# Kernel tuning notes

Measured on AMD Instinct MI355X. Metric: run time of the kernel, lower is better.

The kernel has to match this reference:

```python
import jax, jax.numpy as jnp
import numpy as np

D_MODEL = 1024
N_HEADS = 16
D_K = D_MODEL // N_HEADS
B, L = 2, 2048


def setup_inputs() -> dict:
    key = jax.random.key(0)
    ks = jax.random.split(key, 13)
    s = 0.02
    inp = {
        'query': jax.random.normal(ks[0], (B, L, D_MODEL), jnp.float32),
        'key': jax.random.normal(ks[1], (B, L, D_MODEL), jnp.float32),
        'value': jax.random.normal(ks[2], (B, L, D_MODEL), jnp.float32),
        'mask': jax.random.randint(ks[3], (1, 1, L, L), 0, 2).astype(bool),
        'W_q': jax.random.normal(ks[4], (D_MODEL, D_MODEL), jnp.float32) * s,
        'b_q': jnp.zeros((D_MODEL,), jnp.float32),
        'W_k': jax.random.normal(ks[5], (D_MODEL, D_MODEL), jnp.float32) * s,
        'b_k': jnp.zeros((D_MODEL,), jnp.float32),
        'W_v': jax.random.normal(ks[6], (D_MODEL, D_MODEL), jnp.float32) * s,
        'b_v': jnp.zeros((D_MODEL,), jnp.float32),
        'W_o': jax.random.normal(ks[7], (D_MODEL, D_MODEL), jnp.float32) * s,
        'b_o': jnp.zeros((D_MODEL,), jnp.float32),
    }
    return inp


def _split_heads(x):
    b, l, _ = x.shape
    return x.reshape(b, l, N_HEADS, D_K).transpose(0, 2, 1, 3)  # [B,H,L,dk]


def reference(query, key, value, mask, W_q, b_q, W_k, b_k, W_v, b_v, W_o, b_o):
    q = _split_heads(query @ W_q + b_q)
    k = _split_heads(key @ W_k + b_k)
    v = _split_heads(value @ W_v + b_v)
    # Unscaled attention logits [B,H,L,L] (NO 1/sqrt(dk))
    logits = jnp.einsum('bhqd,bhkd->bhqk', q, k)
    logits = jnp.where(mask, -jnp.inf, logits)
    w = jax.nn.softmax(logits, axis=-1)
    w = jnp.nan_to_num(w, nan=0.0)  # fully-masked rows -> zeros
    attended = jnp.einsum('bhqk,bhkd->bhqd', w, v)
    # dropout in eval mode = identity; combine heads
    out = attended.transpose(0, 2, 1, 3).reshape(B, L, D_MODEL)
    return out @ W_o + b_o
```

## Files before the change

### kernel.cpp

```cpp
#include <hip/hip_runtime.h>
#include <hip/hip_bf16.h>
#include <stdint.h>


typedef __bf16 bf16;
typedef __bf16 bf16x8 __attribute__((ext_vector_type(8)));
typedef float f32x4 __attribute__((ext_vector_type(4)));

#define AS1 __attribute__((address_space(1)))
#define AS3 __attribute__((address_space(3)))

__device__ __forceinline__ void g2l16(const void* g, void* l) {
    __builtin_amdgcn_global_load_lds((AS1 void*)g, (AS3 void*)l, 16, 0, 0);
}

__device__ __forceinline__ bool lane_masked(unsigned long long m) {
#if __has_builtin(__builtin_amdgcn_inverse_ballot_w64)
    return __builtin_amdgcn_inverse_ballot_w64(m);
#else
    return (m >> (threadIdx.x & 63)) & 1ull;
#endif
}

#define LOG2E 1.44269504088896f

__global__ __launch_bounds__(256) void cvt3_kernel(const float* __restrict__ a0,
                                                   const float* __restrict__ a1,
                                                   const float* __restrict__ a2,
                                                   bf16* o0, bf16* o1, bf16* o2) {
    int y = blockIdx.y;
    const float* in = (y == 0) ? a0 : (y == 1) ? a1 : a2;
    bf16* out = (y == 0) ? o0 : (y == 1) ? o1 : o2;
    int idx = blockIdx.x * 256 + threadIdx.x;
    float4 v = ((const float4*)in)[idx];
    __align__(8) bf16 o[4];
    o[0] = (bf16)v.x; o[1] = (bf16)v.y; o[2] = (bf16)v.z; o[3] = (bf16)v.w;
    *(uint2*)(out + (size_t)idx * 4) = *(const uint2*)o;
}

__global__ __launch_bounds__(256) void mdetect_kernel(const unsigned int* __restrict__ w,
                                                      int* __restrict__ flag) {
    int idx = blockIdx.x * 256 + threadIdx.x;
    unsigned v = w[idx];
    int f = 0;
    if (v == 0x3F800000u) f = 2;
    else if (v > 1u) f = 1;
    unsigned long long b1 = __ballot(f & 1);
    unsigned long long b2 = __ballot(f & 2);
    if ((threadIdx.x & 63) == 0) {
        int agg = (b1 ? 1 : 0) | (b2 ? 2 : 0);
        if (agg) atomicOr(flag, agg);
    }
}

__global__ __launch_bounds__(256) void mpack_kernel(const void* __restrict__ mask,
                                                    unsigned long long* __restrict__ mb,
                                                    const int* __restrict__ flag) {
    int idx = blockIdx.x * 256 + threadIdx.x;
    int f = *flag;
    bool v;
    if (f & 2)      v = ((const float*)mask)[idx] != 0.0f;
    else if (f & 1) v = ((const unsigned char*)mask)[idx] != 0;
    else            v = ((const int*)mask)[idx] != 0;
    unsigned long long b = __ballot(v);
    if ((threadIdx.x & 63) == 0) mb[idx >> 6] = b;
}

__global__ __launch_bounds__(256) void rpack_kernel(const unsigned long long* __restrict__ mb,
                                                    unsigned long long* __restrict__ rmb) {
    int task = blockIdx.x * 4 + (threadIdx.x >> 6);
    int qg = task >> 5, kt = task & 31;
    int lane = threadIdx.x & 63, quad = lane >> 4, col = lane & 15;
    #pragma unroll
    for (int r = 0; r < 4; ++r) {
        unsigned long long wrow = mb[(size_t)(qg * 16 + quad * 4 + r) * 32 + kt];
        #pragma unroll
        for (int nt = 0; nt < 4; ++nt) {
            unsigned long long b = __ballot(((wrow >> (nt * 16 + col)) & 1ull) != 0);
            if (lane == 0) rmb[(size_t)task * 16 + r * 4 + nt] = b;
        }
    }
}

__global__ __launch_bounds__(256) void wtrans_kernel(const float* W0, const float* W1,
                                                     const float* W2, const float* W3,
                                                     bf16* T0, bf16* T1, bf16* T2, bf16* T3) {
    const float* W; bf16* T;
    int y = blockIdx.y;
    if (y == 0)      { W = W0; T = T0; }
    else if (y == 1) { W = W1; T = T1; }
    else if (y == 2) { W = W2; T = T2; }
    else             { W = W3; T = T3; }
    int tx = blockIdx.x & 15, ty = blockIdx.x >> 4;
    int n0 = tx * 64, k0 = ty * 64;
    __shared__ __align__(16) bf16 t[64 * 72];
    int tid = threadIdx.x;
    #pragma unroll
    for (int rr = 0; rr < 4; ++rr) {
        int idx = rr * 256 + tid;
        int r = idx >> 4, c4 = (idx & 15) * 4;
        float4 v = *(const float4*)(W + (size_t)(k0 + r) * 1024 + n0 + c4);
        __align__(8) bf16 o[4];
        o[0] = (bf16)v.x; o[1] = (bf16)v.y; o[2] = (bf16)v.z; o[3] = (bf16)v.w;
        *(uint2*)&t[r * 72 + c4] = *(const uint2*)o;
    }
    __syncthreads();
    #pragma unroll
    for (int rr = 0; rr < 2; ++rr) {
        int idx = rr * 256 + tid;
        int n = idx >> 3, kc = (idx & 7) * 8;
        __align__(16) bf16 o[8];
        #pragma unroll
        for (int j = 0; j < 8; ++j) o[j] = t[(kc + j) * 72 + n];
        *(uint4*)(T + (size_t)(n0 + n) * 1024 + k0 + kc) = *(const uint4*)o;
    }
}

template <int MODE>
__device__ __forceinline__ void gemm128_core(const bf16* __restrict__ A,
                                             const bf16* __restrict__ Bt,
                                             const float* __restrict__ bias,
                                             void* __restrict__ Out, int bm, int bn,
                                             float scale) {
    __shared__ __align__(16) bf16 la[128 * 32];
    __shared__ __align__(16) bf16 lb[128 * 32];
    int tid = threadIdx.x;
    int w = tid >> 6, lane = tid & 63;
    int quad = lane >> 4, col = lane & 15;
    int wm = w >> 1, wn = w & 1;
    int m0 = bm * 128, n0 = bn * 128;
    f32x4 acc[4][4];
    f32x4 z = {0.f, 0.f, 0.f, 0.f};
    #pragma unroll
    for (int i = 0; i < 4; ++i)
        #pragma unroll
        for (int j = 0; j < 4; ++j) acc[i][j] = z;
    int srow = lane >> 2;
    int skc = (lane & 3) * 8;
    for (int kt = 0; kt < 32; ++kt) {
        int kk = kt * 32;
        __syncthreads();
        #pragma unroll
        for (int rr = 0; rr < 2; ++rr) {
            int ch = rr * 4 + w;
            int row = ch * 16 + srow;
            g2l16(A + (size_t)(m0 + row) * 1024 + kk + skc, &la[ch * 512]);
            g2l16(Bt + (size_t)(n0 + row) * 1024 + kk + skc, &lb[ch * 512]);
        }
        __syncthreads();
        bf16x8 af[4], bfr[4];
        #pragma unroll
        for (int mt = 0; mt < 4; ++mt)
            af[mt] = *(const bf16x8*)&la[(wm * 64 + mt * 16 + col) * 32 + quad * 8];
        #pragma unroll
        for (int nt = 0; nt < 4; ++nt)
            bfr[nt] = *(const bf16x8*)&lb[(wn * 64 + nt * 16 + col) * 32 + quad * 8];
        #pragma unroll
        for (int mt = 0; mt < 4; ++mt)
            #pragma unroll
            for (int nt = 0; nt < 4; ++nt)
                acc[mt][nt] = __builtin_amdgcn_mfma_f32_16x16x32_bf16(
                    af[mt], bfr[nt], acc[mt][nt], 0, 0, 0);
    }
    float bia[4];
    #pragma unroll
    for (int nt = 0; nt < 4; ++nt) bia[nt] = bias[n0 + wn * 64 + nt * 16 + col];
    #pragma unroll
    for (int mt = 0; mt < 4; ++mt) {
        #pragma unroll
        for (int nt = 0; nt < 4; ++nt) {
            #pragma unroll
            for (int r = 0; r < 4; ++r) {
                int m = m0 + wm * 64 + mt * 16 + quad * 4 + r;
                int n = n0 + wn * 64 + nt * 16 + col;
                float v = (acc[mt][nt][r] + bia[nt]) * scale;
                if (MODE == 0) {
                    int b = m >> 11, l = m & 2047, h = n >> 6, d = n & 63;
                    ((bf16*)Out)[(((size_t)b * 16 + h) * 2048 + l) * 64 + d] = (bf16)v;
                } else {
                    int b = m >> 11, l = m & 2047, h = n >> 6, d = n & 63;
                    ((bf16*)Out)[(((size_t)b * 16 + h) * 64 + d) * 2048 + l] = (bf16)v;
                }
            }
        }
    }
}

__global__ __launch_bounds__(256) void qkv_kernel(
    const bf16* Xq, const bf16* Xk, const bf16* Xv,
    const bf16* Wq, const bf16* Wk, const bf16* Wv,
    const float* bq, const float* bk, const float* bv,
    bf16* Qh, bf16* Kh, bf16* Vt) {
    int y = blockIdx.y;
    int bm = blockIdx.x >> 3, bn = blockIdx.x & 7;
    if (y == 0)      gemm128_core<0>(Xq, Wq, bq, Qh, bm, bn, LOG2E);
    else if (y == 1) gemm128_core<0>(Xk, Wk, bk, Kh, bm, bn, 1.0f);
    else             gemm128_core<2>(Xv, Wv, bv, Vt, bm, bn, 1.0f);
}

__global__ __launch_bounds__(256) void ogemm_kernel(const bf16* __restrict__ A,
                                                    const bf16* __restrict__ Wt,
                                                    const float* __restrict__ bias,
                                                    float* __restrict__ Out) {
    int bm = blockIdx.x >> 3, bn = blockIdx.x & 7;
    __shared__ __align__(16) bf16 la[64 * 32];
    __shared__ __align__(16) bf16 lb[128 * 32];
    int tid = threadIdx.x;
    int w = tid >> 6, lane = tid & 63;
    int quad = lane >> 4, col = lane & 15;
    int m0 = bm * 64, n0 = bn * 128;
    f32x4 acc[4][2];
    f32x4 z = {0.f, 0.f, 0.f, 0.f};
    #pragma unroll
    for (int i = 0; i < 4; ++i) { acc[i][0] = z; acc[i][1] = z; }
    int srow = lane >> 2;
    int skc = (lane & 3) * 8;
    for (int kt = 0; kt < 32; ++kt) {
        int kk = kt * 32;
        __syncthreads();
        g2l16(A + (size_t)(m0 + w * 16 + srow) * 1024 + kk + skc, &la[w * 512]);
        #pragma unroll
        for (int rr = 0; rr < 2; ++rr) {
            int ch = rr * 4 + w;
            g2l16(Wt + (size_t)(n0 + ch * 16 + srow) * 1024 + kk + skc, &lb[ch * 512]);
        }
        __syncthreads();
        bf16x8 af[4], bfr[2];
        #pragma unroll
        for (int mt = 0; mt < 4; ++mt)
            af[mt] = *(const bf16x8*)&la[(mt * 16 + col) * 32 + quad * 8];
        #pragma unroll
        for (int nt = 0; nt < 2; ++nt)
            bfr[nt] = *(const bf16x8*)&lb[(w * 32 + nt * 16 + col) * 32 + quad * 8];
        #pragma unroll
        for (int mt = 0; mt < 4; ++mt)
            #pragma unroll
            for (int nt = 0; nt < 2; ++nt)
                acc[mt][nt] = __builtin_amdgcn_mfma_f32_16x16x32_bf16(
                    af[mt], bfr[nt], acc[mt][nt], 0, 0, 0);
    }
    float bia[2];
    bia[0] = bias[n0 + w * 32 + col];
    bia[1] = bias[n0 + w * 32 + 16 + col];
    #pragma unroll
    for (int mt = 0; mt < 4; ++mt)
        #pragma unroll
        for (int nt = 0; nt < 2; ++nt)
            #pragma unroll
            for (int r = 0; r < 4; ++r)
                Out[(size_t)(m0 + mt * 16 + quad * 4 + r) * 1024 +
                    n0 + w * 32 + nt * 16 + col] = acc[mt][nt][r] + bia[nt];
}

__global__ __launch_bounds__(128) void attn_kernel(const bf16* __restrict__ Qh,
                                                   const bf16* __restrict__ Kh,
                                                   const bf16* __restrict__ Vt,
                                                   const unsigned long long* __restrict__ rmb,
                                                   bf16* __restrict__ att) {
    int bh = blockIdx.x, qt = blockIdx.y;
    int b = bh >> 4, h = bh & 15;
    int q0 = qt * 64;
    __shared__ __align__(16) bf16 ks[64 * 64];
    __shared__ __align__(16) bf16 vs[64 * 64];
    __shared__ __align__(16) bf16 ps[2 * 32 * 72];
    int tid = threadIdx.x;
    int w = tid >> 6, lane = tid & 63;
    int quad = lane >> 4, col = lane & 15;
    int c7 = col & 7;
    int sr = lane >> 3;
    int sg = (lane & 7) ^ sr;
    int swz0 = (quad ^ c7) * 8;
    int swz1 = ((4 + quad) ^ c7) * 8;

    int mofs = __builtin_amdgcn_readfirstlane((qt * 4 + w * 2) * 512);

    #pragma unroll
    for (int i = 0; i < 4; ++i) {
        int ch = w * 4 + i;
        g2l16(Qh + ((size_t)bh * 2048 + q0 + ch * 8 + sr) * 64 + sg * 8, &ks[ch * 512]);
    }
    __syncthreads();
    bf16x8 aq[2][2];
    #pragma unroll
    for (int mt = 0; mt < 2; ++mt) {
        aq[mt][0] = *(const bf16x8*)&ks[(w * 32 + mt * 16 + col) * 64 + swz0];
        aq[mt][1] = *(const bf16x8*)&ks[(w * 32 + mt * 16 + col) * 64 + swz1];
    }
    bf16x8 onesf;
    #pragma unroll
    for (int i = 0; i < 8; ++i) onesf[i] = (bf16)1.0f;

    f32x4 z = {0.f, 0.f, 0.f, 0.f};
    f32x4 O[2][4], R[2];
    #pragma unroll
    for (int mt = 0; mt < 2; ++mt) {
        R[mt] = z;
        #pragma unroll
        for (int i = 0; i < 4; ++i) O[mt][i] = z;
    }

    for (int kt = 0; kt < 32; ++kt) {
        __syncthreads();
        #pragma unroll
        for (int i = 0; i < 4; ++i) {
            int ch = w * 4 + i;
            int r = ch * 8 + sr;
            g2l16(Kh + ((size_t)bh * 2048 + kt * 64 + r) * 64 + sg * 8, &ks[ch * 512]);
            g2l16(Vt + ((size_t)bh * 64 + r) * 2048 + kt * 64 + sg * 8, &vs[ch * 512]);
        }
        __syncthreads();

        f32x4 s[2][4];
        #pragma unroll
        for (int nt = 0; nt < 4; ++nt) {
            s[0][nt] = z; s[1][nt] = z;
            bf16x8 bk0 = *(const bf16x8*)&ks[(nt * 16 + col) * 64 + swz0];
            s[0][nt] = __builtin_amdgcn_mfma_f32_16x16x32_bf16(aq[0][0], bk0, s[0][nt], 0, 0, 0);
            s[1][nt] = __builtin_amdgcn_mfma_f32_16x16x32_bf16(aq[1][0], bk0, s[1][nt], 0, 0, 0);
            bf16x8 bk1 = *(const bf16x8*)&ks[(nt * 16 + col) * 64 + swz1];
            s[0][nt] = __builtin_amdgcn_mfma_f32_16x16x32_bf16(aq[0][1], bk1, s[0][nt], 0, 0, 0);
            s[1][nt] = __builtin_amdgcn_mfma_f32_16x16x32_bf16(aq[1][1], bk1, s[1][nt], 0, 0, 0);
        }

        #pragma unroll
        for (int mt = 0; mt < 2; ++mt) {
            const unsigned long long* mw = rmb + mofs + mt * 512 + kt * 16;
            #pragma unroll
            for (int r = 0; r < 4; ++r) {
                #pragma unroll
                for (int nt = 0; nt < 4; ++nt) {
                    float p = __builtin_amdgcn_exp2f(s[mt][nt][r]);
                    if (lane_masked(mw[r * 4 + nt])) p = 0.0f;
                    ps[w * 2304 + (mt * 16 + quad * 4 + r) * 72 + nt * 16 + col] = (bf16)p;
                }
            }
        }

        bf16x8 ap[2][2];
        #pragma unroll
        for (int mt = 0; mt < 2; ++mt) {
            ap[mt][0] = *(const bf16x8*)&ps[w * 2304 + (mt * 16 + col) * 72 + quad * 8];
            ap[mt][1] = *(const bf16x8*)&ps[w * 2304 + (mt * 16 + col) * 72 + 32 + quad * 8];
        }
        #pragma unroll
        for (int dt = 0; dt < 4; ++dt) {
            bf16x8 bv0 = *(const bf16x8*)&vs[(dt * 16 + col) * 64 + swz0];
            O[0][dt] = __builtin_amdgcn_mfma_f32_16x16x32_bf16(ap[0][0], bv0, O[0][dt], 0, 0, 0);
            O[1][dt] = __builtin_amdgcn_mfma_f32_16x16x32_bf16(ap[1][0], bv0, O[1][dt], 0, 0, 0);
            bf16x8 bv1 = *(const bf16x8*)&vs[(dt * 16 + col) * 64 + swz1];
            O[0][dt] = __builtin_amdgcn_mfma_f32_16x16x32_bf16(ap[0][1], bv1, O[0][dt], 0, 0, 0);
            O[1][dt] = __builtin_amdgcn_mfma_f32_16x16x32_bf16(ap[1][1], bv1, O[1][dt], 0, 0, 0);
        }
        #pragma unroll
        for (int mt = 0; mt < 2; ++mt) {
            R[mt] = __builtin_amdgcn_mfma_f32_16x16x32_bf16(ap[mt][0], onesf, R[mt], 0, 0, 0);
            R[mt] = __builtin_amdgcn_mfma_f32_16x16x32_bf16(ap[mt][1], onesf, R[mt], 0, 0, 0);
        }
    }

    #pragma unroll
    for (int mt = 0; mt < 2; ++mt) {
        #pragma unroll
        for (int r = 0; r < 4; ++r) {
            float rsv = R[mt][r];
            float inv = (rsv > 0.f) ? 1.0f / rsv : 0.f;
            int qg = q0 + w * 32 + mt * 16 + quad * 4 + r;
            #pragma unroll
            for (int dt = 0; dt < 4; ++dt) {
                float ov = O[mt][dt][r] * inv;
                att[((size_t)b * 2048 + qg) * 1024 + h * 64 + dt * 16 + col] = (bf16)ov;
            }
        }
    }
}

extern "C" void kernel_launch(void* const* d_in, const int* in_sizes, int n_in,
                              void* d_out, int out_size, void* d_ws, size_t ws_size,
                              hipStream_t stream) {
    (void)in_sizes; (void)n_in; (void)out_size; (void)ws_size;
    const float* query = (const float*)d_in[0];
    const float* key_  = (const float*)d_in[1];
    const float* value = (const float*)d_in[2];
    const void*  mask  = d_in[3];
    const float* W_q = (const float*)d_in[4];
    const float* b_q = (const float*)d_in[5];
    const float* W_k = (const float*)d_in[6];
    const float* b_k = (const float*)d_in[7];
    const float* W_v = (const float*)d_in[8];
    const float* b_v = (const float*)d_in[9];
    const float* W_o = (const float*)d_in[10];
    const float* b_o = (const float*)d_in[11];

    char* ws = (char*)d_ws;
    bf16* Xq  = (bf16*)(ws + 0);
    bf16* Xk  = (bf16*)(ws + 8388608);
    bf16* Xv  = (bf16*)(ws + 16777216);
    bf16* Wtq = (bf16*)(ws + 25165824);
    bf16* Wtk = (bf16*)(ws + 27262976);
    bf16* Wtv = (bf16*)(ws + 29360128);
    bf16* Wto = (bf16*)(ws + 31457280);
    bf16* Qh  = (bf16*)(ws + 33554432);
    bf16* Kh  = (bf16*)(ws + 41943040);
    bf16* Vt  = (bf16*)(ws + 50331648);
    bf16* att = (bf16*)(ws + 58720256);
    unsigned long long* mb  = (unsigned long long*)(ws + 67108864);
    unsigned long long* rmb = (unsigned long long*)(ws + 67633152);
    int* flag = (int*)(ws + 68157440);

    hipMemsetAsync(flag, 0, 4, stream);
    mdetect_kernel<<<4096, 256, 0, stream>>>((const unsigned int*)mask, flag);
    mpack_kernel<<<16384, 256, 0, stream>>>(mask, mb, flag);
    rpack_kernel<<<1024, 256, 0, stream>>>(mb, rmb);

    cvt3_kernel<<<dim3(4096, 3), 256, 0, stream>>>(query, key_, value, Xq, Xk, Xv);
    wtrans_kernel<<<dim3(256, 4), 256, 0, stream>>>(W_q, W_k, W_v, W_o, Wtq, Wtk, Wtv, Wto);

    qkv_kernel<<<dim3(256, 3), 256, 0, stream>>>(Xq, Xk, Xv, Wtq, Wtk, Wtv,
                                                 b_q, b_k, b_v, Qh, Kh, Vt);
    attn_kernel<<<dim3(32, 32), 128, 0, stream>>>(Qh, Kh, Vt, rmb, att);
    ogemm_kernel<<<512, 256, 0, stream>>>(att, Wto, b_o, (float*)d_out);
}
```

Baseline: 274.3 us.

## Split attention key range across two wave pairs and merge partial results in LDS

The attention kernel now runs 256 threads per block. Two halves of the block each process half of the key sequence in 32-key tiles, and their partial O and row-sum accumulators are reduced through shared memory at the end. The aim is more waves per block and more latency hiding for the same grid size, which doubles the parallelism along the key dimension. In exchange it adds a final LDS reduction, smaller per-iteration tiles with more barriers per unit of work, and changed V tile swizzling and mask indexing.

```diff
diff --git a/kernel.cpp b/kernel.cpp
--- a/kernel.cpp
+++ b/kernel.cpp
@@ -252,7 +252,7 @@
                     n0 + w * 32 + nt * 16 + col] = acc[mt][nt][r] + bia[nt];
 }
 
-__global__ __launch_bounds__(128) void attn_kernel(const bf16* __restrict__ Qh,
+__global__ __launch_bounds__(256) void attn_kernel(const bf16* __restrict__ Qh,
                                                    const bf16* __restrict__ Kh,
                                                    const bf16* __restrict__ Vt,
                                                    const unsigned long long* __restrict__ rmb,
@@ -260,31 +260,34 @@
     int bh = blockIdx.x, qt = blockIdx.y;
     int b = bh >> 4, h = bh & 15;
     int q0 = qt * 64;
-    __shared__ __align__(16) bf16 ks[64 * 64];
-    __shared__ __align__(16) bf16 vs[64 * 64];
-    __shared__ __align__(16) bf16 ps[2 * 32 * 72];
+    __shared__ __align__(16) bf16 kv[2][2][32 * 64];
+    __shared__ __align__(16) bf16 ps[4][32 * 36];
     int tid = threadIdx.x;
     int w = tid >> 6, lane = tid & 63;
+    int half = w >> 1, wq = w & 1;
     int quad = lane >> 4, col = lane & 15;
-    int c7 = col & 7;
+    int c7 = col & 7, c3 = col & 3;
     int sr = lane >> 3;
     int sg = (lane & 7) ^ sr;
+    int vr = lane >> 2;
+    int vg = (lane & 3) ^ (vr & 3);
     int swz0 = (quad ^ c7) * 8;
     int swz1 = ((4 + quad) ^ c7) * 8;
 
-    int mofs = __builtin_amdgcn_readfirstlane((qt * 4 + w * 2) * 512);
-
-    #pragma unroll
-    for (int i = 0; i < 4; ++i) {
-        int ch = w * 4 + i;
-        g2l16(Qh + ((size_t)bh * 2048 + q0 + ch * 8 + sr) * 64 + sg * 8, &ks[ch * 512]);
+    int mofs = __builtin_amdgcn_readfirstlane((qt * 4 + wq * 2) * 512);
+
+    bf16* qb = &kv[0][0][0];
+    #pragma unroll
+    for (int i = 0; i < 2; ++i) {
+        int ch = w * 2 + i;
+        g2l16(Qh + ((size_t)bh * 2048 + q0 + ch * 8 + sr) * 64 + sg * 8, qb + ch * 512);
     }
     __syncthreads();
     bf16x8 aq[2][2];
     #pragma unroll
     for (int mt = 0; mt < 2; ++mt) {
-        aq[mt][0] = *(const bf16x8*)&ks[(w * 32 + mt * 16 + col) * 64 + swz0];
-        aq[mt][1] = *(const bf16x8*)&ks[(w * 32 + mt * 16 + col) * 64 + swz1];
+        aq[mt][0] = *(const bf16x8*)&qb[(wq * 32 + mt * 16 + col) * 64 + swz0];
+        aq[mt][1] = *(const bf16x8*)&qb[(wq * 32 + mt * 16 + col) * 64 + swz1];
     }
     bf16x8 onesf;
     #pragma unroll
@@ -299,76 +302,93 @@
         for (int i = 0; i < 4; ++i) O[mt][i] = z;
     }
 
-    for (int kt = 0; kt < 32; ++kt) {
-        __syncthreads();
-        #pragma unroll
-        for (int i = 0; i < 4; ++i) {
-            int ch = w * 4 + i;
-            int r = ch * 8 + sr;
-            g2l16(Kh + ((size_t)bh * 2048 + kt * 64 + r) * 64 + sg * 8, &ks[ch * 512]);
-            g2l16(Vt + ((size_t)bh * 64 + r) * 2048 + kt * 64 + sg * 8, &vs[ch * 512]);
-        }
-        __syncthreads();
-
-        f32x4 s[2][4];
-        #pragma unroll
-        for (int nt = 0; nt < 4; ++nt) {
+    bf16* ksb = &kv[half][0][0];
+    bf16* vsb = &kv[half][1][0];
+    for (int it = 0; it < 32; ++it) {
+        int kt = half * 32 + it;
+        __syncthreads();
+        #pragma unroll
+        for (int i = 0; i < 2; ++i) {
+            int ch = wq * 2 + i;
+            g2l16(Kh + ((size_t)bh * 2048 + kt * 32 + ch * 8 + sr) * 64 + sg * 8,
+                  ksb + ch * 512);
+            g2l16(Vt + ((size_t)bh * 64 + ch * 16 + vr) * 2048 + kt * 32 + vg * 8,
+                  vsb + ch * 512);
+        }
+        __syncthreads();
+
+        f32x4 s[2][2];
+        #pragma unroll
+        for (int nt = 0; nt < 2; ++nt) {
             s[0][nt] = z; s[1][nt] = z;
-            bf16x8 bk0 = *(const bf16x8*)&ks[(nt * 16 + col) * 64 + swz0];
+            bf16x8 bk0 = *(const bf16x8*)&ksb[(nt * 16 + col) * 64 + swz0];
             s[0][nt] = __builtin_amdgcn_mfma_f32_16x16x32_bf16(aq[0][0], bk0, s[0][nt], 0, 0, 0);
             s[1][nt] = __builtin_amdgcn_mfma_f32_16x16x32_bf16(aq[1][0], bk0, s[1][nt], 0, 0, 0);
-            bf16x8 bk1 = *(const bf16x8*)&ks[(nt * 16 + col) * 64 + swz1];
+            bf16x8 bk1 = *(const bf16x8*)&ksb[(nt * 16 + col) * 64 + swz1];
             s[0][nt] = __builtin_amdgcn_mfma_f32_16x16x32_bf16(aq[0][1], bk1, s[0][nt], 0, 0, 0);
             s[1][nt] = __builtin_amdgcn_mfma_f32_16x16x32_bf16(aq[1][1], bk1, s[1][nt], 0, 0, 0);
         }
 
         #pragma unroll
         for (int mt = 0; mt < 2; ++mt) {
-            const unsigned long long* mw = rmb + mofs + mt * 512 + kt * 16;
+            const unsigned long long* mw =
+                rmb + mofs + mt * 512 + (kt >> 1) * 16 + (kt & 1) * 2;
             #pragma unroll
             for (int r = 0; r < 4; ++r) {
                 #pragma unroll
-                for (int nt = 0; nt < 4; ++nt) {
+                for (int nt = 0; nt < 2; ++nt) {
                     float p = __builtin_amdgcn_exp2f(s[mt][nt][r]);
                     if (lane_masked(mw[r * 4 + nt])) p = 0.0f;
-                    ps[w * 2304 + (mt * 16 + quad * 4 + r) * 72 + nt * 16 + col] = (bf16)p;
+                    ps[w][(mt * 16 + quad * 4 + r) * 36 + nt * 16 + col] = (bf16)p;
                 }
             }
         }
 
-        bf16x8 ap[2][2];
+        bf16x8 ap[2];
+        ap[0] = *(const bf16x8*)&ps[w][(col) * 36 + quad * 8];
+        ap[1] = *(const bf16x8*)&ps[w][(16 + col) * 36 + quad * 8];
+        #pragma unroll
+        for (int dt = 0; dt < 4; ++dt) {
+            bf16x8 bv = *(const bf16x8*)&vsb[(dt * 16 + col) * 32 + (quad ^ c3) * 8];
+            O[0][dt] = __builtin_amdgcn_mfma_f32_16x16x32_bf16(ap[0], bv, O[0][dt], 0, 0, 0);
+            O[1][dt] = __builtin_amdgcn_mfma_f32_16x16x32_bf16(ap[1], bv, O[1][dt], 0, 0, 0);
+        }
+        R[0] = __builtin_amdgcn_mfma_f32_16x16x32_bf16(ap[0], onesf, R[0], 0, 0, 0);
+        R[1] = __builtin_amdgcn_mfma_f32_16x16x32_bf16(ap[1], onesf, R[1], 0, 0, 0);
+    }
+
+    __syncthreads();
+    float* obuf = (float*)&kv[0][0][0];
+    float* rbuf = (float*)&ps[0][0];
+    if (half == 1) {
         #pragma unroll
         for (int mt = 0; mt < 2; ++mt) {
-            ap[mt][0] = *(const bf16x8*)&ps[w * 2304 + (mt * 16 + col) * 72 + quad * 8];
-            ap[mt][1] = *(const bf16x8*)&ps[w * 2304 + (mt * 16 + col) * 72 + 32 + quad * 8];
-        }
-        #pragma unroll
-        for (int dt = 0; dt < 4; ++dt) {
-            bf16x8 bv0 = *(const bf16x8*)&vs[(dt * 16 + col) * 64 + swz0];
-            O[0][dt] = __builtin_amdgcn_mfma_f32_16x16x32_bf16(ap[0][0], bv0, O[0][dt], 0, 0, 0);
-            O[1][dt] = __builtin_amdgcn_mfma_f32_16x16x32_bf16(ap[1][0], bv0, O[1][dt], 0, 0, 0);
-            bf16x8 bv1 = *(const bf16x8*)&vs[(dt * 16 + col) * 64 + swz1];
-            O[0][dt] = __builtin_amdgcn_mfma_f32_16x16x32_bf16(ap[0][1], bv1, O[0][dt], 0, 0, 0);
-            O[1][dt] = __builtin_amdgcn_mfma_f32_16x16x32_bf16(ap[1][1], bv1, O[1][dt], 0, 0, 0);
-        }
+            #pragma unroll
+            for (int r = 0; r < 4; ++r) {
+                int row = mt * 16 + quad * 4 + r;
+                #pragma unroll
+                for (int dt = 0; dt < 4; ++dt)
+                    obuf[(size_t)wq * 2048 + row * 64 + dt * 16 + col] = O[mt][dt][r];
+                if (col == 0) rbuf[wq * 32 + row] = R[mt][r];
+            }
+        }
+    }
+    __syncthreads();
+    if (half == 0) {
         #pragma unroll
         for (int mt = 0; mt < 2; ++mt) {
-            R[mt] = __builtin_amdgcn_mfma_f32_16x16x32_bf16(ap[mt][0], onesf, R[mt], 0, 0, 0);
-            R[mt] = __builtin_amdgcn_mfma_f32_16x16x32_bf16(ap[mt][1], onesf, R[mt], 0, 0, 0);
-        }
-    }
-
-    #pragma unroll
-    for (int mt = 0; mt < 2; ++mt) {
-        #pragma unroll
-        for (int r = 0; r < 4; ++r) {
-            float rsv = R[mt][r];
-            float inv = (rsv > 0.f) ? 1.0f / rsv : 0.f;
-            int qg = q0 + w * 32 + mt * 16 + quad * 4 + r;
-            #pragma unroll
-            for (int dt = 0; dt < 4; ++dt) {
-                float ov = O[mt][dt][r] * inv;
-                att[((size_t)b * 2048 + qg) * 1024 + h * 64 + dt * 16 + col] = (bf16)ov;
+            #pragma unroll
+            for (int r = 0; r < 4; ++r) {
+                int row = mt * 16 + quad * 4 + r;
+                float rsv = R[mt][r] + rbuf[wq * 32 + row];
+                float inv = (rsv > 0.f) ? 1.0f / rsv : 0.f;
+                int qg = q0 + wq * 32 + row;
+                #pragma unroll
+                for (int dt = 0; dt < 4; ++dt) {
+                    float ov = (O[mt][dt][r] +
+                                obuf[(size_t)wq * 2048 + row * 64 + dt * 16 + col]) * inv;
+                    att[((size_t)b * 2048 + qg) * 1024 + h * 64 + dt * 16 + col] = (bf16)ov;
+                }
             }
         }
     }
@@ -417,6 +437,6 @@
 
     qkv_kernel<<<dim3(256, 3), 256, 0, stream>>>(Xq, Xk, Xv, Wtq, Wtk, Wtv,
                                                  b_q, b_k, b_v, Qh, Kh, Vt);
-    attn_kernel<<<dim3(32, 32), 128, 0, stream>>>(Qh, Kh, Vt, rmb, att);
+    attn_kernel<<<dim3(32, 32), 256, 0, stream>>>(Qh, Kh, Vt, rmb, att);
     ogemm_kernel<<<512, 256, 0, stream>>>(att, Wto, b_o, (float*)d_out);
 }
```

Measured after the change: 333.2 us. 21.5% more time.

## Double-buffer K/V tiles in attention and swizzle the P scratch tile

Applied to the files above, without the earlier changes.

The attention loop now uses two LDS buffers for K and V. It issues the global-to-LDS loads for the next key tile before running the QK and PV MFMAs on the current one, and drops one barrier per iteration, so load latency can overlap with compute. The per-wave P tile loses its row padding and uses an XOR swizzle that matches the MFMA operand read pattern, to avoid LDS bank conflicts. The cost is more LDS per block, which may lower occupancy, plus one wasted prefetch (of tile 0) on the last iteration.

```diff
diff --git a/kernel.cpp b/kernel.cpp
--- a/kernel.cpp
+++ b/kernel.cpp
@@ -260,9 +260,11 @@
     int bh = blockIdx.x, qt = blockIdx.y;
     int b = bh >> 4, h = bh & 15;
     int q0 = qt * 64;
-    __shared__ __align__(16) bf16 ks[64 * 64];
-    __shared__ __align__(16) bf16 vs[64 * 64];
-    __shared__ __align__(16) bf16 ps[2 * 32 * 72];
+    __shared__ __align__(16) bf16 kA[64 * 64];
+    __shared__ __align__(16) bf16 vA[64 * 64];
+    __shared__ __align__(16) bf16 kB[64 * 64];
+    __shared__ __align__(16) bf16 vB[64 * 64];
+    __shared__ __align__(16) bf16 ps[2][32 * 64];
     int tid = threadIdx.x;
     int w = tid >> 6, lane = tid & 63;
     int quad = lane >> 4, col = lane & 15;
@@ -277,14 +279,14 @@
     #pragma unroll
     for (int i = 0; i < 4; ++i) {
         int ch = w * 4 + i;
-        g2l16(Qh + ((size_t)bh * 2048 + q0 + ch * 8 + sr) * 64 + sg * 8, &ks[ch * 512]);
+        g2l16(Qh + ((size_t)bh * 2048 + q0 + ch * 8 + sr) * 64 + sg * 8, &kA[ch * 512]);
     }
     __syncthreads();
     bf16x8 aq[2][2];
     #pragma unroll
     for (int mt = 0; mt < 2; ++mt) {
-        aq[mt][0] = *(const bf16x8*)&ks[(w * 32 + mt * 16 + col) * 64 + swz0];
-        aq[mt][1] = *(const bf16x8*)&ks[(w * 32 + mt * 16 + col) * 64 + swz1];
+        aq[mt][0] = *(const bf16x8*)&kA[(w * 32 + mt * 16 + col) * 64 + swz0];
+        aq[mt][1] = *(const bf16x8*)&kA[(w * 32 + mt * 16 + col) * 64 + swz1];
     }
     bf16x8 onesf;
     #pragma unroll
@@ -299,39 +301,50 @@
         for (int i = 0; i < 4; ++i) O[mt][i] = z;
     }
 
-    for (int kt = 0; kt < 32; ++kt) {
+    __syncthreads();
+    #pragma unroll
+    for (int i = 0; i < 4; ++i) {
+        int ch = w * 4 + i;
+        int r = ch * 8 + sr;
+        g2l16(Kh + ((size_t)bh * 2048 + r) * 64 + sg * 8, &kA[ch * 512]);
+        g2l16(Vt + ((size_t)bh * 64 + r) * 2048 + sg * 8, &vA[ch * 512]);
+    }
+
+    auto body = [&](const bf16* RDk, const bf16* RDv, bf16* WRk, bf16* WRv, int t) {
         __syncthreads();
+        int ktn = (t + 1) & 31;
         #pragma unroll
         for (int i = 0; i < 4; ++i) {
             int ch = w * 4 + i;
             int r = ch * 8 + sr;
-            g2l16(Kh + ((size_t)bh * 2048 + kt * 64 + r) * 64 + sg * 8, &ks[ch * 512]);
-            g2l16(Vt + ((size_t)bh * 64 + r) * 2048 + kt * 64 + sg * 8, &vs[ch * 512]);
-        }
-        __syncthreads();
+            g2l16(Kh + ((size_t)bh * 2048 + ktn * 64 + r) * 64 + sg * 8, WRk + ch * 512);
+            g2l16(Vt + ((size_t)bh * 64 + r) * 2048 + ktn * 64 + sg * 8, WRv + ch * 512);
+        }
 
         f32x4 s[2][4];
         #pragma unroll
         for (int nt = 0; nt < 4; ++nt) {
             s[0][nt] = z; s[1][nt] = z;
-            bf16x8 bk0 = *(const bf16x8*)&ks[(nt * 16 + col) * 64 + swz0];
+            bf16x8 bk0 = *(const bf16x8*)&RDk[(nt * 16 + col) * 64 + swz0];
             s[0][nt] = __builtin_amdgcn_mfma_f32_16x16x32_bf16(aq[0][0], bk0, s[0][nt], 0, 0, 0);
             s[1][nt] = __builtin_amdgcn_mfma_f32_16x16x32_bf16(aq[1][0], bk0, s[1][nt], 0, 0, 0);
-            bf16x8 bk1 = *(const bf16x8*)&ks[(nt * 16 + col) * 64 + swz1];
+            bf16x8 bk1 = *(const bf16x8*)&RDk[(nt * 16 + col) * 64 + swz1];
             s[0][nt] = __builtin_amdgcn_mfma_f32_16x16x32_bf16(aq[0][1], bk1, s[0][nt], 0, 0, 0);
             s[1][nt] = __builtin_amdgcn_mfma_f32_16x16x32_bf16(aq[1][1], bk1, s[1][nt], 0, 0, 0);
         }
 
         #pragma unroll
         for (int mt = 0; mt < 2; ++mt) {
-            const unsigned long long* mw = rmb + mofs + mt * 512 + kt * 16;
+            const unsigned long long* mw = rmb + mofs + mt * 512 + t * 16;
             #pragma unroll
             for (int r = 0; r < 4; ++r) {
+                int row = mt * 16 + quad * 4 + r;
+                int xr = (quad * 4 + r) & 7;
                 #pragma unroll
                 for (int nt = 0; nt < 4; ++nt) {
                     float p = __builtin_amdgcn_exp2f(s[mt][nt][r]);
                     if (lane_masked(mw[r * 4 + nt])) p = 0.0f;
-                    ps[w * 2304 + (mt * 16 + quad * 4 + r) * 72 + nt * 16 + col] = (bf16)p;
+                    ps[w][row * 64 + ((nt * 16 + col) ^ (xr << 3))] = (bf16)p;
                 }
             }
         }
@@ -339,15 +352,15 @@
         bf16x8 ap[2][2];
         #pragma unroll
         for (int mt = 0; mt < 2; ++mt) {
-            ap[mt][0] = *(const bf16x8*)&ps[w * 2304 + (mt * 16 + col) * 72 + quad * 8];
-            ap[mt][1] = *(const bf16x8*)&ps[w * 2304 + (mt * 16 + col) * 72 + 32 + quad * 8];
+            ap[mt][0] = *(const bf16x8*)&ps[w][(mt * 16 + col) * 64 + swz0];
+            ap[mt][1] = *(const bf16x8*)&ps[w][(mt * 16 + col) * 64 + swz1];
         }
         #pragma unroll
         for (int dt = 0; dt < 4; ++dt) {
-            bf16x8 bv0 = *(const bf16x8*)&vs[(dt * 16 + col) * 64 + swz0];
+            bf16x8 bv0 = *(const bf16x8*)&RDv[(dt * 16 + col) * 64 + swz0];
             O[0][dt] = __builtin_amdgcn_mfma_f32_16x16x32_bf16(ap[0][0], bv0, O[0][dt], 0, 0, 0);
             O[1][dt] = __builtin_amdgcn_mfma_f32_16x16x32_bf16(ap[1][0], bv0, O[1][dt], 0, 0, 0);
-            bf16x8 bv1 = *(const bf16x8*)&vs[(dt * 16 + col) * 64 + swz1];
+            bf16x8 bv1 = *(const bf16x8*)&RDv[(dt * 16 + col) * 64 + swz1];
             O[0][dt] = __builtin_amdgcn_mfma_f32_16x16x32_bf16(ap[0][1], bv1, O[0][dt], 0, 0, 0);
             O[1][dt] = __builtin_amdgcn_mfma_f32_16x16x32_bf16(ap[1][1], bv1, O[1][dt], 0, 0, 0);
         }
@@ -356,6 +369,11 @@
             R[mt] = __builtin_amdgcn_mfma_f32_16x16x32_bf16(ap[mt][0], onesf, R[mt], 0, 0, 0);
             R[mt] = __builtin_amdgcn_mfma_f32_16x16x32_bf16(ap[mt][1], onesf, R[mt], 0, 0, 0);
         }
+    };
+
+    for (int t2 = 0; t2 < 16; ++t2) {
+        body(kA, vA, kB, vB, t2 * 2);
+        body(kB, vB, kA, vA, t2 * 2 + 1);
     }
 
     #pragma unroll
```

Result: slower. 290.6 us (+5.9%).

## Split attention KV range across waves and load K/V directly into registers

Applied to the files above, without the earlier changes.

Each wave now handles all 64 query rows of the block but only half of the key sequence, a split-K scheme. The two waves' partial O and row sums are combined through shared memory at the end. K and V tiles are read straight from global memory into registers instead of being staged in LDS, which removes the per-tile __syncthreads barriers. In exchange, register pressure roughly doubles, global loads are no longer coalesced through LDS, and a final reduction step is added.

```diff
diff --git a/kernel.cpp b/kernel.cpp
--- a/kernel.cpp
+++ b/kernel.cpp
@@ -260,115 +260,130 @@
     int bh = blockIdx.x, qt = blockIdx.y;
     int b = bh >> 4, h = bh & 15;
     int q0 = qt * 64;
-    __shared__ __align__(16) bf16 ks[64 * 64];
-    __shared__ __align__(16) bf16 vs[64 * 64];
-    __shared__ __align__(16) bf16 ps[2 * 32 * 72];
+    __shared__ __align__(16) bf16 ps[2][64 * 64];
+    __shared__ float rbuf[64];
     int tid = threadIdx.x;
     int w = tid >> 6, lane = tid & 63;
-    int quad = lane >> 4, col = lane & 15;
-    int c7 = col & 7;
-    int sr = lane >> 3;
-    int sg = (lane & 7) ^ sr;
+    int quad = lane >> 4, col = lane & 15, c7 = col & 7;
     int swz0 = (quad ^ c7) * 8;
     int swz1 = ((4 + quad) ^ c7) * 8;
 
-    int mofs = __builtin_amdgcn_readfirstlane((qt * 4 + w * 2) * 512);
-
-    #pragma unroll
-    for (int i = 0; i < 4; ++i) {
-        int ch = w * 4 + i;
-        g2l16(Qh + ((size_t)bh * 2048 + q0 + ch * 8 + sr) * 64 + sg * 8, &ks[ch * 512]);
-    }
-    __syncthreads();
-    bf16x8 aq[2][2];
-    #pragma unroll
-    for (int mt = 0; mt < 2; ++mt) {
-        aq[mt][0] = *(const bf16x8*)&ks[(w * 32 + mt * 16 + col) * 64 + swz0];
-        aq[mt][1] = *(const bf16x8*)&ks[(w * 32 + mt * 16 + col) * 64 + swz1];
+    const bf16* qp = Qh + ((size_t)bh * 2048 + q0) * 64;
+    bf16x8 aq[4][2];
+    #pragma unroll
+    for (int mt = 0; mt < 4; ++mt) {
+        aq[mt][0] = *(const bf16x8*)(qp + (mt * 16 + col) * 64 + quad * 8);
+        aq[mt][1] = *(const bf16x8*)(qp + (mt * 16 + col) * 64 + 32 + quad * 8);
     }
     bf16x8 onesf;
     #pragma unroll
     for (int i = 0; i < 8; ++i) onesf[i] = (bf16)1.0f;
 
     f32x4 z = {0.f, 0.f, 0.f, 0.f};
-    f32x4 O[2][4], R[2];
-    #pragma unroll
-    for (int mt = 0; mt < 2; ++mt) {
+    f32x4 O[4][4], R[4];
+    #pragma unroll
+    for (int mt = 0; mt < 4; ++mt) {
         R[mt] = z;
         #pragma unroll
-        for (int i = 0; i < 4; ++i) O[mt][i] = z;
-    }
-
-    for (int kt = 0; kt < 32; ++kt) {
-        __syncthreads();
-        #pragma unroll
-        for (int i = 0; i < 4; ++i) {
-            int ch = w * 4 + i;
-            int r = ch * 8 + sr;
-            g2l16(Kh + ((size_t)bh * 2048 + kt * 64 + r) * 64 + sg * 8, &ks[ch * 512]);
-            g2l16(Vt + ((size_t)bh * 64 + r) * 2048 + kt * 64 + sg * 8, &vs[ch * 512]);
-        }
-        __syncthreads();
-
-        f32x4 s[2][4];
+        for (int dt = 0; dt < 4; ++dt) O[mt][dt] = z;
+    }
+
+    int mofs = __builtin_amdgcn_readfirstlane(qt * 2048 + w * 256);
+
+    const bf16* kbase = Kh + ((size_t)bh * 2048 + w * 16 * 64) * 64;
+    const bf16* vbase = Vt + (size_t)bh * 64 * 2048 + w * 16 * 64;
+    bf16* myps = &ps[w][0];
+
+    #pragma unroll 2
+    for (int t = 0; t < 16; ++t) {
+        bf16x8 bv[4][2];
+        #pragma unroll
+        for (int dt = 0; dt < 4; ++dt) {
+            const bf16* vp = vbase + (size_t)(dt * 16 + col) * 2048 + t * 64;
+            bv[dt][0] = *(const bf16x8*)(vp + quad * 8);
+            bv[dt][1] = *(const bf16x8*)(vp + 32 + quad * 8);
+        }
+        const bf16* kp = kbase + t * 4096;
+        bf16x8 bk[4][2];
         #pragma unroll
         for (int nt = 0; nt < 4; ++nt) {
-            s[0][nt] = z; s[1][nt] = z;
-            bf16x8 bk0 = *(const bf16x8*)&ks[(nt * 16 + col) * 64 + swz0];
-            s[0][nt] = __builtin_amdgcn_mfma_f32_16x16x32_bf16(aq[0][0], bk0, s[0][nt], 0, 0, 0);
-            s[1][nt] = __builtin_amdgcn_mfma_f32_16x16x32_bf16(aq[1][0], bk0, s[1][nt], 0, 0, 0);
-            bf16x8 bk1 = *(const bf16x8*)&ks[(nt * 16 + col) * 64 + swz1];
-            s[0][nt] = __builtin_amdgcn_mfma_f32_16x16x32_bf16(aq[0][1], bk1, s[0][nt], 0, 0, 0);
-            s[1][nt] = __builtin_amdgcn_mfma_f32_16x16x32_bf16(aq[1][1], bk1, s[1][nt], 0, 0, 0);
-        }
-
-        #pragma unroll
-        for (int mt = 0; mt < 2; ++mt) {
-            const unsigned long long* mw = rmb + mofs + mt * 512 + kt * 16;
+            bk[nt][0] = *(const bf16x8*)(kp + (nt * 16 + col) * 64 + quad * 8);
+            bk[nt][1] = *(const bf16x8*)(kp + (nt * 16 + col) * 64 + 32 + quad * 8);
+        }
+
+        #pragma unroll
+        for (int mt = 0; mt < 4; ++mt) {
+            f32x4 s[4];
+            #pragma unroll
+            for (int nt = 0; nt < 4; ++nt) {
+                s[nt] = z;
+                s[nt] = __builtin_amdgcn_mfma_f32_16x16x32_bf16(aq[mt][0], bk[nt][0], s[nt], 0, 0, 0);
+                s[nt] = __builtin_amdgcn_mfma_f32_16x16x32_bf16(aq[mt][1], bk[nt][1], s[nt], 0, 0, 0);
+            }
+            const unsigned long long* mw = rmb + mofs + mt * 512 + t * 16;
             #pragma unroll
             for (int r = 0; r < 4; ++r) {
+                int row = mt * 16 + quad * 4 + r;
+                int xs = ((quad * 4 + r) & 7) << 3;
                 #pragma unroll
                 for (int nt = 0; nt < 4; ++nt) {
-                    float p = __builtin_amdgcn_exp2f(s[mt][nt][r]);
+                    float p = __builtin_amdgcn_exp2f(s[nt][r]);
                     if (lane_masked(mw[r * 4 + nt])) p = 0.0f;
-                    ps[w * 2304 + (mt * 16 + quad * 4 + r) * 72 + nt * 16 + col] = (bf16)p;
+                    myps[row * 64 + ((nt * 16 + col) ^ xs)] = (bf16)p;
                 }
             }
         }
 
-        bf16x8 ap[2][2];
-        #pragma unroll
-        for (int mt = 0; mt < 2; ++mt) {
-            ap[mt][0] = *(const bf16x8*)&ps[w * 2304 + (mt * 16 + col) * 72 + quad * 8];
-            ap[mt][1] = *(const bf16x8*)&ps[w * 2304 + (mt * 16 + col) * 72 + 32 + quad * 8];
-        }
-        #pragma unroll
-        for (int dt = 0; dt < 4; ++dt) {
-            bf16x8 bv0 = *(const bf16x8*)&vs[(dt * 16 + col) * 64 + swz0];
-            O[0][dt] = __builtin_amdgcn_mfma_f32_16x16x32_bf16(ap[0][0], bv0, O[0][dt], 0, 0, 0);
-            O[1][dt] = __builtin_amdgcn_mfma_f32_16x16x32_bf16(ap[1][0], bv0, O[1][dt], 0, 0, 0);
-            bf16x8 bv1 = *(const bf16x8*)&vs[(dt * 16 + col) * 64 + swz1];
-            O[0][dt] = __builtin_amdgcn_mfma_f32_16x16x32_bf16(ap[0][1], bv1, O[0][dt], 0, 0, 0);
-            O[1][dt] = __builtin_amdgcn_mfma_f32_16x16x32_bf16(ap[1][1], bv1, O[1][dt], 0, 0, 0);
-        }
-        #pragma unroll
-        for (int mt = 0; mt < 2; ++mt) {
+        bf16x8 ap[4][2];
+        #pragma unroll
+        for (int mt = 0; mt < 4; ++mt) {
+            ap[mt][0] = *(const bf16x8*)&myps[(mt * 16 + col) * 64 + swz0];
+            ap[mt][1] = *(const bf16x8*)&myps[(mt * 16 + col) * 64 + swz1];
+        }
+        #pragma unroll
+        for (int dt = 0; dt < 4; ++dt)
+            #pragma unroll
+            for (int mt = 0; mt < 4; ++mt) {
+                O[mt][dt] = __builtin_amdgcn_mfma_f32_16x16x32_bf16(ap[mt][0], bv[dt][0], O[mt][dt], 0, 0, 0);
+                O[mt][dt] = __builtin_amdgcn_mfma_f32_16x16x32_bf16(ap[mt][1], bv[dt][1], O[mt][dt], 0, 0, 0);
+            }
+        #pragma unroll
+        for (int mt = 0; mt < 4; ++mt) {
             R[mt] = __builtin_amdgcn_mfma_f32_16x16x32_bf16(ap[mt][0], onesf, R[mt], 0, 0, 0);
             R[mt] = __builtin_amdgcn_mfma_f32_16x16x32_bf16(ap[mt][1], onesf, R[mt], 0, 0, 0);
         }
     }
 
-    #pragma unroll
-    for (int mt = 0; mt < 2; ++mt) {
-        #pragma unroll
-        for (int r = 0; r < 4; ++r) {
-            float rsv = R[mt][r];
-            float inv = (rsv > 0.f) ? 1.0f / rsv : 0.f;
-            int qg = q0 + w * 32 + mt * 16 + quad * 4 + r;
-            #pragma unroll
-            for (int dt = 0; dt < 4; ++dt) {
-                float ov = O[mt][dt][r] * inv;
-                att[((size_t)b * 2048 + qg) * 1024 + h * 64 + dt * 16 + col] = (bf16)ov;
+    __syncthreads();
+    float* obuf = (float*)&ps[0][0];
+    if (w == 1) {
+        #pragma unroll
+        for (int mt = 0; mt < 4; ++mt) {
+            #pragma unroll
+            for (int r = 0; r < 4; ++r) {
+                int row = mt * 16 + quad * 4 + r;
+                #pragma unroll
+                for (int dt = 0; dt < 4; ++dt)
+                    obuf[row * 64 + dt * 16 + col] = O[mt][dt][r];
+                if (col == 0) rbuf[row] = R[mt][r];
+            }
+        }
+    }
+    __syncthreads();
+    if (w == 0) {
+        #pragma unroll
+        for (int mt = 0; mt < 4; ++mt) {
+            #pragma unroll
+            for (int r = 0; r < 4; ++r) {
+                int row = mt * 16 + quad * 4 + r;
+                float rsv = R[mt][r] + rbuf[row];
+                float inv = (rsv > 0.f) ? 1.0f / rsv : 0.f;
+                int qg = q0 + row;
+                #pragma unroll
+                for (int dt = 0; dt < 4; ++dt) {
+                    float ov = (O[mt][dt][r] + obuf[row * 64 + dt * 16 + col]) * inv;
+                    att[((size_t)b * 2048 + qg) * 1024 + h * 64 + dt * 16 + col] = (bf16)ov;
+                }
             }
         }
     }
```

Measured after the change: 333.4 us. 1.22x slower.
